# Kernel tuning notes

Hardware: AMD Instinct MI355X
Metric: run time of the kernel (lower is better)

## Reference

```python
import jax, jax.numpy as jnp
import numpy as np
import math

_B, _L, _D, _H = 4, 2048, 512, 8
_DH = _D // _H


def setup_inputs() -> dict:
    key = jax.random.key(0)
    ks = jax.random.split(key, 16)
    w_scale = 1.0 / math.sqrt(_D)
    def lin(kw, kb):
        W = jax.random.uniform(kw, (_D, _D), jnp.float32, -w_scale, w_scale)
        b = jax.random.uniform(kb, (_D,), jnp.float32, -w_scale, w_scale)
        return W, b
    Wq_w, Wq_b = lin(ks[0], ks[1])
    Wk_w, Wk_b = lin(ks[2], ks[3])
    Wv_w, Wv_b = lin(ks[4], ks[5])
    fc_w, fc_b = lin(ks[6], ks[7])
    Q = jax.random.normal(ks[8], (_B, _L, _D), jnp.float32)
    K = jax.random.normal(ks[9], (_B, _L, _D), jnp.float32)
    V = jax.random.normal(ks[10], (_B, _L, _D), jnp.float32)
    # E = torch.rand(L, DH): uniform [0,1), non-trainable buffer
    E = jax.random.uniform(ks[11], (_L, _DH), jnp.float32)
    # causal mask: True (1) where attention is disallowed -> gets -1e9
    mask = jnp.triu(jnp.ones((_L, _L), dtype=bool), k=1)[None, None]  # (1,1,L,L)
    return {"Q": Q, "K": K, "V": V, "mask": mask,
            "Wq_w": Wq_w, "Wq_b": Wq_b, "Wk_w": Wk_w, "Wk_b": Wk_b,
            "Wv_w": Wv_w, "Wv_b": Wv_b, "fc_w": fc_w, "fc_b": fc_b,
            "E": E, "H": _H}


def reference(Q, K, V, mask, Wq_w, Wq_b, Wk_w, Wk_b, Wv_w, Wv_b, fc_w, fc_b, E, H):
    B, Lq, D = Q.shape
    DH = D // H

    def proj(x, W, b):  # torch Linear: x @ W.T + b, then split heads -> (B,H,L,DH)
        y = x @ W.T + b
        return y.reshape(B, -1, H, DH).transpose(0, 2, 1, 3)

    q = proj(Q, Wq_w, Wq_b)
    k = proj(K, Wk_w, Wk_b)
    v = proj(V, Wv_w, Wv_b)
    Lk = k.shape[2]

    # _get_left_embedding: last Lq rows of E
    Eu = E[max(0, E.shape[0] - Lq):, :]            # (e, DH), e == Lq here
    e = Eu.shape[0]

    QE = jnp.einsum('bhld,ed->bhle', q, Eu)        # (B,H,Lq,e)
    # _qe_masking: keep QE[..., i, j] where j >= e-1-i (upper anti-triangle)
    i = jnp.arange(Lq)[:, None]
    j = jnp.arange(e)[None, :]
    keep = (i + j >= e - 1).astype(QE.dtype)
    QE = QE * keep

    # _skewing: pad one zero column, reshape, drop first row
    padded = jnp.pad(QE, ((0, 0), (0, 0), (0, 0), (1, 0)))   # (B,H,Lq,e+1)
    Srel = padded.reshape(B, H, e + 1, Lq)[:, :, 1:, :]      # (B,H,e,Lq)
    if Lk < Lq:
        Srel = Srel[:, :, :, :Lk]

    logits = (jnp.einsum('bhld,bhmd->bhlm', q, k) + Srel) / math.sqrt(DH)
    logits = logits + mask.astype(jnp.float32) * (-1e9)
    AW = jax.nn.softmax(logits, axis=-1)
    out = jnp.einsum('bhlm,bhmd->bhld', AW, v)               # (B,H,Lq,DH)
    out = out.transpose(0, 2, 1, 3).reshape(B, -1, D)        # (B,Lq,D)
    return out @ fc_w.T + fc_b
```

## Files before the change

### kernel.cpp

```cpp
#include <hip/hip_runtime.h>
#include <stdint.h>

typedef __bf16 bf16;
typedef float f32x4 __attribute__((ext_vector_type(4)));
typedef bf16 bf16x8 __attribute__((ext_vector_type(8)));
typedef bf16 bf16x4 __attribute__((ext_vector_type(4)));

#define MFMA16(a, b, c) __builtin_amdgcn_mfma_f32_16x16x32_bf16((a), (b), (c), 0, 0, 0)
#define EXP2F(x) __builtin_amdgcn_exp2f(x)

__device__ __forceinline__ void gll16(const void* g, void* l) {
  __builtin_amdgcn_global_load_lds((const __attribute__((address_space(1))) void*)g,
                                   (__attribute__((address_space(3))) void*)l, 16, 0, 0);
}

__global__ __launch_bounds__(256) void convert_all(
    const float4* __restrict__ Q, const float4* __restrict__ K, const float4* __restrict__ V,
    const float4* __restrict__ Wq, const float4* __restrict__ Wk, const float4* __restrict__ Wv,
    const float4* __restrict__ fcw, const float4* __restrict__ E,
    bf16x4* __restrict__ Xq, bf16x4* __restrict__ Xk, bf16x4* __restrict__ Xv,
    bf16x4* __restrict__ Wqb, bf16x4* __restrict__ Wkb, bf16x4* __restrict__ Wvb,
    bf16x4* __restrict__ fcb, bf16x4* __restrict__ Eb) {
  int i = blockIdx.x * 256 + threadIdx.x;
  const float4* s;
  bf16x4* d;
  int off;
  if (i < 1048576) { s = Q; d = Xq; off = i; }
  else if (i < 2097152) { s = K; d = Xk; off = i - 1048576; }
  else if (i < 3145728) { s = V; d = Xv; off = i - 2097152; }
  else if (i < 3211264) { s = Wq; d = Wqb; off = i - 3145728; }
  else if (i < 3276800) { s = Wk; d = Wkb; off = i - 3211264; }
  else if (i < 3342336) { s = Wv; d = Wvb; off = i - 3276800; }
  else if (i < 3407872) { s = fcw; d = fcb; off = i - 3342336; }
  else { s = E; d = Eb; off = i - 3407872; }
  float4 v = s[off];
  bf16x4 o;
  o[0] = (bf16)v.x; o[1] = (bf16)v.y; o[2] = (bf16)v.z; o[3] = (bf16)v.w;
  d[off] = o;
}

__device__ __forceinline__ void gemm_core(const bf16* __restrict__ A, const bf16* __restrict__ Bt,
                                          bf16* ldsA, bf16* ldsB, int m0, int n0,
                                          f32x4 acc[4][4]) {
  const int t = threadIdx.x;
  const int lane = t & 63, w = t >> 6;
  const int l15 = lane & 15, quad = lane >> 4;
  const int wm = w >> 1, wn = w & 1;
#pragma unroll
  for (int i = 0; i < 4; i++)
#pragma unroll
    for (int j = 0; j < 4; j++) acc[i][j] = (f32x4){0.f, 0.f, 0.f, 0.f};

  const int ch0 = t, ch1 = t + 256;
  const int r0 = ch0 >> 2, c0 = (ch0 & 3) ^ (r0 & 3);
  const int r1 = ch1 >> 2, c1 = (ch1 & 3) ^ (r1 & 3);

  int aoff[4], boff[4];
#pragma unroll
  for (int mt = 0; mt < 4; mt++) {
    int m = wm * 64 + mt * 16 + l15;
    aoff[mt] = (m << 6) + ((quad ^ (l15 & 3)) << 4);
    int n = wn * 64 + mt * 16 + l15;
    boff[mt] = (n << 6) + ((quad ^ (l15 & 3)) << 4);
  }
  bf16* ldsA1 = ldsA + w * 512;
  bf16* ldsA2 = ldsA + 2048 + w * 512;
  bf16* ldsB1 = ldsB + w * 512;
  bf16* ldsB2 = ldsB + 2048 + w * 512;

  for (int kt = 0; kt < 512; kt += 32) {
    gll16(A + (size_t)(m0 + r0) * 512 + kt + c0 * 8, ldsA1);
    gll16(A + (size_t)(m0 + r1) * 512 + kt + c1 * 8, ldsA2);
    gll16(Bt + (size_t)(n0 + r0) * 512 + kt + c0 * 8, ldsB1);
    gll16(Bt + (size_t)(n0 + r1) * 512 + kt + c1 * 8, ldsB2);
    __syncthreads();
    bf16x8 af[4], bfr[4];
#pragma unroll
    for (int mt = 0; mt < 4; mt++) af[mt] = *(const bf16x8*)((const char*)ldsA + aoff[mt]);
#pragma unroll
    for (int nt = 0; nt < 4; nt++) bfr[nt] = *(const bf16x8*)((const char*)ldsB + boff[nt]);
#pragma unroll
    for (int mt = 0; mt < 4; mt++)
#pragma unroll
      for (int nt = 0; nt < 4; nt++)
        acc[mt][nt] = MFMA16(af[mt], bfr[nt], acc[mt][nt]);
    __syncthreads();
  }
}

__global__ __launch_bounds__(256) void proj_gemm(
    const bf16* __restrict__ Xq, const bf16* __restrict__ Xk, const bf16* __restrict__ Xv,
    const bf16* __restrict__ Wq, const bf16* __restrict__ Wk, const bf16* __restrict__ Wv,
    const float* __restrict__ bq, const float* __restrict__ bk, const float* __restrict__ bv,
    bf16* __restrict__ qb, bf16* __restrict__ kb, bf16* __restrict__ vb) {
  __shared__ bf16 ldsA[128 * 32];
  __shared__ bf16 ldsB[128 * 32];
  const int z = blockIdx.z;
  const bf16* A = z == 0 ? Xq : (z == 1 ? Xk : Xv);
  const bf16* W = z == 0 ? Wq : (z == 1 ? Wk : Wv);
  const float* bias = z == 0 ? bq : (z == 1 ? bk : bv);
  bf16* out = z == 0 ? qb : (z == 1 ? kb : vb);
  const int m0 = blockIdx.x * 128, n0 = blockIdx.y * 128;
  f32x4 acc[4][4];
  gemm_core(A, W, ldsA, ldsB, m0, n0, acc);

  const int t = threadIdx.x;
  const int lane = t & 63, w = t >> 6;
  const int l15 = lane & 15, quad = lane >> 4;
  const int wm = w >> 1, wn = w & 1;
#pragma unroll
  for (int mt = 0; mt < 4; mt++)
#pragma unroll
    for (int nt = 0; nt < 4; nt++)
#pragma unroll
      for (int r = 0; r < 4; r++) {
        int gm = m0 + wm * 64 + mt * 16 + quad * 4 + r;
        int gn = n0 + wn * 64 + nt * 16 + l15;
        float v = acc[mt][nt][r] + bias[gn];
        int b = gm >> 11, l = gm & 2047, h = gn >> 6, d = gn & 63;
        out[(((size_t)(b * 8 + h)) * 2048 + l) * 64 + d] = (bf16)v;
      }
}

__global__ __launch_bounds__(256) void final_gemm(const bf16* __restrict__ A,
                                                  const bf16* __restrict__ W,
                                                  const float* __restrict__ bias,
                                                  float* __restrict__ out) {
  __shared__ bf16 ldsA[128 * 32];
  __shared__ bf16 ldsB[128 * 32];
  const int m0 = blockIdx.x * 128, n0 = blockIdx.y * 128;
  f32x4 acc[4][4];
  gemm_core(A, W, ldsA, ldsB, m0, n0, acc);

  const int t = threadIdx.x;
  const int lane = t & 63, w = t >> 6;
  const int l15 = lane & 15, quad = lane >> 4;
  const int wm = w >> 1, wn = w & 1;
#pragma unroll
  for (int mt = 0; mt < 4; mt++)
#pragma unroll
    for (int nt = 0; nt < 4; nt++)
#pragma unroll
      for (int r = 0; r < 4; r++) {
        int gm = m0 + wm * 64 + mt * 16 + quad * 4 + r;
        int gn = n0 + wn * 64 + nt * 16 + l15;
        out[(size_t)gm * 512 + gn] = acc[mt][nt][r] + bias[gn];
      }
}

__global__ __launch_bounds__(256) void transpose_v(const bf16* __restrict__ vbuf,
                                                   bf16* __restrict__ vT) {
  __shared__ bf16 tile[64][72];
  const int bh = blockIdx.y, l0 = blockIdx.x * 64;
  const bf16* src = vbuf + ((size_t)bh * 2048 + l0) * 64;
  bf16* dst = vT + (size_t)bh * 64 * 2048 + l0;
  const int t = threadIdx.x;
#pragma unroll
  for (int p = 0; p < 2; p++) {
    int ch = t + p * 256;
    int r = ch >> 3, c8 = ch & 7;
    *(bf16x8*)&tile[r][c8 * 8] = *(const bf16x8*)&src[(size_t)r * 64 + c8 * 8];
  }
  __syncthreads();
#pragma unroll
  for (int p = 0; p < 2; p++) {
    int ch = t + p * 256;
    int dr = ch >> 3, lc = ch & 7;
    bf16x8 v;
#pragma unroll
    for (int j = 0; j < 8; j++) v[j] = tile[lc * 8 + j][dr];
    *(bf16x8*)&dst[(size_t)dr * 2048 + lc * 8] = v;
  }
}

__global__ __launch_bounds__(256, 4) void attn_kernel(
    const bf16* __restrict__ qbuf, const bf16* __restrict__ kbuf,
    const bf16* __restrict__ vT, const bf16* __restrict__ Eb,
    bf16* __restrict__ attnb, bf16* __restrict__ Of1,
    float* __restrict__ Os0, float* __restrict__ Os1) {
  __shared__ bf16 Kl[64 * 64];
  __shared__ bf16 Vl[64 * 64];
  __shared__ bf16 Pl[4][16 * 72];
  const int t = threadIdx.x, w = t >> 6, lane = t & 63;
  const int l15 = lane & 15, quad = lane >> 4;
  const int x = blockIdx.x;
  const int bh = x & 31, job = x >> 5;
  int strip, jt0, jt1;
  bool isB;
  if (job < 16) {
    strip = 16 + job; jt0 = 0; jt1 = 16; isB = false;
  } else {
    int k = job - 16, i = k >> 1;
    if ((k & 1) == 0) { strip = 15 - i; jt0 = 0; jt1 = 16 - i; isB = false; }
    else { strip = 31 - i; jt0 = 16; jt1 = 32 - i; isB = true; }
  }
  const int i0 = strip * 64 + w * 16;
  bf16* Pw = Pl[w];
  const bf16* qh = qbuf + (size_t)bh * 2048 * 64;
  const bf16* kh = kbuf + (size_t)bh * 2048 * 64;
  const bf16* vh = vT + (size_t)bh * 64 * 2048;

  const int sr0 = t >> 3, sc0 = (t & 7) ^ (sr0 & 7);
  const int sr1 = sr0 + 32;
  const int wb0 = (t & 192) * 16;
  const int wb1 = 4096 + wb0;

  int bpaddr[4];
  bool loA[4];
#pragma unroll
  for (int r = 0; r < 4; r++) {
    int u = quad * 4 + r;
    bpaddr[r] = (((l15 + 15 - u) & 15) + 16 * quad) * 4;
    loA[r] = (l15 <= u);
  }

  bf16x8 aq0, aq1;
  {
    const bf16* qrow = qh + (size_t)(i0 + l15) * 64 + quad * 8;
    aq0 = *(const bf16x8*)qrow;
    aq1 = *(const bf16x8*)(qrow + 32);
  }
  bf16x8 ones;
#pragma unroll
  for (int j = 0; j < 8; j++) ones[j] = (bf16)1.0f;

  f32x4 O[4], Osum;
  Osum = (f32x4){0.f, 0.f, 0.f, 0.f};
#pragma unroll
  for (int i = 0; i < 4; i++) O[i] = (f32x4){0.f, 0.f, 0.f, 0.f};
  const float sc = 0.125f * 1.44269504088896f;
  const int ebase00 = 2047 - i0 - 15;

  float Bpc[4];
  {
    int er = ebase00 + jt0 * 64 + l15;
    er = er > 2047 ? 2047 : er;
    const bf16* erow = Eb + (size_t)er * 64 + quad * 8;
    bf16x8 e0 = *(const bf16x8*)erow;
    bf16x8 e1 = *(const bf16x8*)(erow + 32);
    f32x4 zz = (f32x4){0.f, 0.f, 0.f, 0.f};
    zz = MFMA16(aq0, e0, zz);
    zz = MFMA16(aq1, e1, zz);
#pragma unroll
    for (int r = 0; r < 4; r++)
      Bpc[r] = __int_as_float(__builtin_amdgcn_ds_bpermute(bpaddr[r], __float_as_int(zz[r])));
  }

  for (int jt = jt0; jt < jt1; jt++) {
    const int j0 = jt * 64;
    const bool diag = (jt == strip);
    __syncthreads();
    gll16(kh + (size_t)(j0 + sr0) * 64 + sc0 * 8, (char*)Kl + wb0);
    gll16(kh + (size_t)(j0 + sr1) * 64 + sc0 * 8, (char*)Kl + wb1);
    gll16(vh + (size_t)sr0 * 2048 + j0 + sc0 * 8, (char*)Vl + wb0);
    gll16(vh + (size_t)sr1 * 2048 + j0 + sc0 * 8, (char*)Vl + wb1);
    float Bp[5][4];
#pragma unroll
    for (int r = 0; r < 4; r++) Bp[0][r] = Bpc[r];
    const int ebase = ebase00 + j0;
#pragma unroll
    for (int nt = 1; nt < 5; nt++) {
      int er = ebase + nt * 16 + l15;
      er = er > 2047 ? 2047 : er;
      const bf16* erow = Eb + (size_t)er * 64 + quad * 8;
      bf16x8 e0 = *(const bf16x8*)erow;
      bf16x8 e1 = *(const bf16x8*)(erow + 32);
      f32x4 zz = (f32x4){0.f, 0.f, 0.f, 0.f};
      zz = MFMA16(aq0, e0, zz);
      zz = MFMA16(aq1, e1, zz);
#pragma unroll
      for (int r = 0; r < 4; r++)
        Bp[nt][r] =
            __int_as_float(__builtin_amdgcn_ds_bpermute(bpaddr[r], __float_as_int(zz[r])));
    }
#pragma unroll
    for (int r = 0; r < 4; r++) Bpc[r] = Bp[4][r];

    __syncthreads();
    f32x4 s[4];
#pragma unroll
    for (int nt = 0; nt < 4; nt++) {
      int row = nt * 16 + l15;
      bf16x8 k0 = *(const bf16x8*)(Kl + ((row << 3) + (quad ^ (row & 7))) * 8);
      bf16x8 k1 = *(const bf16x8*)(Kl + ((row << 3) + ((quad + 4) ^ (row & 7))) * 8);
      f32x4 zz = (f32x4){0.f, 0.f, 0.f, 0.f};
      zz = MFMA16(aq0, k0, zz);
      s[nt] = MFMA16(aq1, k1, zz);
    }
    if (diag) {
#pragma unroll
      for (int nt = 0; nt < 4; nt++)
#pragma unroll
        for (int r = 0; r < 4; r++) {
          int u = quad * 4 + r;
          int j = nt * 16 + l15;
          float skew = loA[r] ? Bp[nt][r] : Bp[nt + 1][r];
          float logit = (s[nt][r] + skew) * sc;
          if (j0 + j > i0 + u) logit = -1e30f;
          Pw[u * 72 + j] = (bf16)EXP2F(logit);
        }
    } else {
#pragma unroll
      for (int nt = 0; nt < 4; nt++)
#pragma unroll
        for (int r = 0; r < 4; r++) {
          int u = quad * 4 + r;
          int j = nt * 16 + l15;
          float skew = loA[r] ? Bp[nt][r] : Bp[nt + 1][r];
          Pw[u * 72 + j] = (bf16)EXP2F((s[nt][r] + skew) * sc);
        }
    }
    bf16x8 pa0 = *(const bf16x8*)&Pw[l15 * 72 + quad * 8];
    bf16x8 pa1 = *(const bf16x8*)&Pw[l15 * 72 + 32 + quad * 8];
    Osum = MFMA16(pa0, ones, Osum);
    Osum = MFMA16(pa1, ones, Osum);
#pragma unroll
    for (int nt = 0; nt < 4; nt++) {
      int row = nt * 16 + l15;
      bf16x8 v0 = *(const bf16x8*)(Vl + ((row << 3) + (quad ^ (row & 7))) * 8);
      bf16x8 v1 = *(const bf16x8*)(Vl + ((row << 3) + ((quad + 4) ^ (row & 7))) * 8);
      O[nt] = MFMA16(pa0, v0, O[nt]);
      O[nt] = MFMA16(pa1, v1, O[nt]);
    }
  }
  if (isB) {
    bf16* orow = Of1 + ((size_t)(bh * 1024 + (i0 - 1024))) * 64;
#pragma unroll
    for (int nt = 0; nt < 4; nt++)
#pragma unroll
      for (int r = 0; r < 4; r++)
        orow[(size_t)(quad * 4 + r) * 64 + nt * 16 + l15] = (bf16)O[nt][r];
    if (l15 == 0) {
#pragma unroll
      for (int r = 0; r < 4; r++) Os1[bh * 1024 + (i0 - 1024) + quad * 4 + r] = Osum[r];
    }
  } else {
    const int b = bh >> 3, hh = bh & 7;
    bf16* orow = attnb + ((size_t)(b * 2048 + i0)) * 512 + hh * 64;
#pragma unroll
    for (int nt = 0; nt < 4; nt++)
#pragma unroll
      for (int r = 0; r < 4; r++)
        orow[(size_t)(quad * 4 + r) * 512 + nt * 16 + l15] = (bf16)O[nt][r];
    if (l15 == 0) {
#pragma unroll
      for (int r = 0; r < 4; r++) Os0[bh * 2048 + i0 + quad * 4 + r] = Osum[r];
    }
  }
}

__global__ __launch_bounds__(256) void norm_kernel(bf16x8* __restrict__ attnb,
                                                   const bf16x8* __restrict__ Of1,
                                                   const float* __restrict__ Os0,
                                                   const float* __restrict__ Os1) {
  int i = blockIdx.x * 256 + threadIdx.x;
  int col8 = i & 63;
  int row = i >> 6;
  int b = row >> 11, l = row & 2047, h = col8 >> 3;
  int bh = b * 8 + h;
  float s = Os0[bh * 2048 + l];
  bf16x8 v0 = attnb[i];
  float acc[8];
#pragma unroll
  for (int j = 0; j < 8; j++) acc[j] = (float)v0[j];
  if (l >= 1024) {
    s += Os1[bh * 1024 + l - 1024];
    bf16x8 v1 = Of1[(size_t)(bh * 1024 + l - 1024) * 8 + (col8 & 7)];
#pragma unroll
    for (int j = 0; j < 8; j++) acc[j] += (float)v1[j];
  }
  float inv = 1.0f / s;
  bf16x8 o;
#pragma unroll
  for (int j = 0; j < 8; j++) o[j] = (bf16)(acc[j] * inv);
  attnb[i] = o;
}

extern "C" void kernel_launch(void* const* d_in, const int* in_sizes, int n_in,
                              void* d_out, int out_size, void* d_ws, size_t ws_size,
                              hipStream_t stream) {
  const float* Q = (const float*)d_in[0];
  const float* K = (const float*)d_in[1];
  const float* V = (const float*)d_in[2];
  const float* Wq = (const float*)d_in[4];
  const float* bq = (const float*)d_in[5];
  const float* Wk = (const float*)d_in[6];
  const float* bk = (const float*)d_in[7];
  const float* Wv = (const float*)d_in[8];
  const float* bv = (const float*)d_in[9];
  const float* fcw = (const float*)d_in[10];
  const float* fcb = (const float*)d_in[11];
  const float* E = (const float*)d_in[12];

  char* ws = (char*)d_ws;
  bf16* Xq = (bf16*)(ws + 0);
  bf16* Xk = (bf16*)(ws + 8388608);
  bf16* Xv = (bf16*)(ws + 16777216);
  bf16* Wqb = (bf16*)(ws + 25165824);
  bf16* Wkb = (bf16*)(ws + 25690112);
  bf16* Wvb = (bf16*)(ws + 26214400);
  bf16* fcwb = (bf16*)(ws + 26738688);
  bf16* Eb = (bf16*)(ws + 27262976);
  bf16* qbuf = (bf16*)(ws + 27525120);
  bf16* kbuf = (bf16*)(ws + 35913728);
  bf16* vbuf = (bf16*)(ws + 44302336);
  bf16* Of1 = (bf16*)(ws + 52690944);
  float* Os0 = (float*)(ws + 56885248);
  float* Os1 = (float*)(ws + 57147392);
  bf16* vTb = Xk;
  bf16* attnb = Xq;

  convert_all<<<13440, 256, 0, stream>>>(
      (const float4*)Q, (const float4*)K, (const float4*)V, (const float4*)Wq,
      (const float4*)Wk, (const float4*)Wv, (const float4*)fcw, (const float4*)E,
      (bf16x4*)Xq, (bf16x4*)Xk, (bf16x4*)Xv, (bf16x4*)Wqb, (bf16x4*)Wkb,
      (bf16x4*)Wvb, (bf16x4*)fcwb, (bf16x4*)Eb);

  proj_gemm<<<dim3(64, 4, 3), 256, 0, stream>>>(Xq, Xk, Xv, Wqb, Wkb, Wvb, bq, bk, bv,
                                                qbuf, kbuf, vbuf);

  transpose_v<<<dim3(32, 32), 256, 0, stream>>>(vbuf, vTb);

  attn_kernel<<<1536, 256, 0, stream>>>(qbuf, kbuf, vTb, Eb, attnb, Of1, Os0, Os1);

  norm_kernel<<<2048, 256, 0, stream>>>((bf16x8*)attnb, (const bf16x8*)Of1, Os0, Os1);

  final_gemm<<<dim3(64, 4, 1), 256, 0, stream>>>(attnb, fcwb, fcb, (float*)d_out);
}
```

Baseline: 247.9 us.

## Fuse fp32-to-bf16 conversion into GEMM tile loads and add MFMA priority hints

The standalone conversion pass over Q, K, V and the weights is removed. The projection and output GEMMs now load fp32 tiles straight into LDS, using a swizzled layout with twice the bytes per tile, and convert to bf16 when reading fragments. This drops a full extra read and write of the activations in exchange for more LDS traffic and conversion work inside the GEMM loop. The attention kernel also raises wave priority around its MFMA sections using s_setprio.

```diff
diff --git a/kernel.cpp b/kernel.cpp
--- a/kernel.cpp
+++ b/kernel.cpp
@@ -14,34 +14,19 @@
                                    (__attribute__((address_space(3))) void*)l, 16, 0, 0);
 }
 
-__global__ __launch_bounds__(256) void convert_all(
-    const float4* __restrict__ Q, const float4* __restrict__ K, const float4* __restrict__ V,
-    const float4* __restrict__ Wq, const float4* __restrict__ Wk, const float4* __restrict__ Wv,
-    const float4* __restrict__ fcw, const float4* __restrict__ E,
-    bf16x4* __restrict__ Xq, bf16x4* __restrict__ Xk, bf16x4* __restrict__ Xv,
-    bf16x4* __restrict__ Wqb, bf16x4* __restrict__ Wkb, bf16x4* __restrict__ Wvb,
-    bf16x4* __restrict__ fcb, bf16x4* __restrict__ Eb) {
+__global__ __launch_bounds__(256) void convert_E(const float4* __restrict__ E,
+                                                 bf16x4* __restrict__ Eb) {
   int i = blockIdx.x * 256 + threadIdx.x;
-  const float4* s;
-  bf16x4* d;
-  int off;
-  if (i < 1048576) { s = Q; d = Xq; off = i; }
-  else if (i < 2097152) { s = K; d = Xk; off = i - 1048576; }
-  else if (i < 3145728) { s = V; d = Xv; off = i - 2097152; }
-  else if (i < 3211264) { s = Wq; d = Wqb; off = i - 3145728; }
-  else if (i < 3276800) { s = Wk; d = Wkb; off = i - 3211264; }
-  else if (i < 3342336) { s = Wv; d = Wvb; off = i - 3276800; }
-  else if (i < 3407872) { s = fcw; d = fcb; off = i - 3342336; }
-  else { s = E; d = Eb; off = i - 3407872; }
-  float4 v = s[off];
+  float4 v = E[i];
   bf16x4 o;
   o[0] = (bf16)v.x; o[1] = (bf16)v.y; o[2] = (bf16)v.z; o[3] = (bf16)v.w;
-  d[off] = o;
-}
-
-__device__ __forceinline__ void gemm_core(const bf16* __restrict__ A, const bf16* __restrict__ Bt,
-                                          bf16* ldsA, bf16* ldsB, int m0, int n0,
-                                          f32x4 acc[4][4]) {
+  Eb[i] = o;
+}
+
+template <bool AF32, bool BF32>
+__device__ __forceinline__ void gemm_core_t(const void* __restrict__ Ap,
+                                            const void* __restrict__ Bp, char* ldsA,
+                                            char* ldsB, int m0, int n0, f32x4 acc[4][4]) {
   const int t = threadIdx.x;
   const int lane = t & 63, w = t >> 6;
   const int l15 = lane & 15, quad = lane >> 4;
@@ -51,34 +36,75 @@
 #pragma unroll
     for (int j = 0; j < 4; j++) acc[i][j] = (f32x4){0.f, 0.f, 0.f, 0.f};
 
-  const int ch0 = t, ch1 = t + 256;
-  const int r0 = ch0 >> 2, c0 = (ch0 & 3) ^ (r0 & 3);
-  const int r1 = ch1 >> 2, c1 = (ch1 & 3) ^ (r1 & 3);
-
-  int aoff[4], boff[4];
-#pragma unroll
-  for (int mt = 0; mt < 4; mt++) {
-    int m = wm * 64 + mt * 16 + l15;
-    aoff[mt] = (m << 6) + ((quad ^ (l15 & 3)) << 4);
-    int n = wn * 64 + mt * 16 + l15;
-    boff[mt] = (n << 6) + ((quad ^ (l15 & 3)) << 4);
-  }
-  bf16* ldsA1 = ldsA + w * 512;
-  bf16* ldsA2 = ldsA + 2048 + w * 512;
-  bf16* ldsB1 = ldsB + w * 512;
-  bf16* ldsB2 = ldsB + 2048 + w * 512;
+  const int wbase = (t & 192) * 16;
 
   for (int kt = 0; kt < 512; kt += 32) {
-    gll16(A + (size_t)(m0 + r0) * 512 + kt + c0 * 8, ldsA1);
-    gll16(A + (size_t)(m0 + r1) * 512 + kt + c1 * 8, ldsA2);
-    gll16(Bt + (size_t)(n0 + r0) * 512 + kt + c0 * 8, ldsB1);
-    gll16(Bt + (size_t)(n0 + r1) * 512 + kt + c1 * 8, ldsB2);
+    if constexpr (AF32) {
+      const float* A = (const float*)Ap;
+#pragma unroll
+      for (int p = 0; p < 4; p++) {
+        int ch = t + 256 * p;
+        int r = ch >> 3, c = (ch & 7) ^ (r & 7);
+        gll16(A + (size_t)(m0 + r) * 512 + kt + c * 4, ldsA + p * 4096 + wbase);
+      }
+    } else {
+      const bf16* A = (const bf16*)Ap;
+#pragma unroll
+      for (int p = 0; p < 2; p++) {
+        int ch = t + 256 * p;
+        int r = ch >> 2, c = (ch & 3) ^ (r & 3);
+        gll16(A + (size_t)(m0 + r) * 512 + kt + c * 8, ldsA + p * 4096 + wbase);
+      }
+    }
+    if constexpr (BF32) {
+      const float* B = (const float*)Bp;
+#pragma unroll
+      for (int p = 0; p < 4; p++) {
+        int ch = t + 256 * p;
+        int r = ch >> 3, c = (ch & 7) ^ (r & 7);
+        gll16(B + (size_t)(n0 + r) * 512 + kt + c * 4, ldsB + p * 4096 + wbase);
+      }
+    } else {
+      const bf16* B = (const bf16*)Bp;
+#pragma unroll
+      for (int p = 0; p < 2; p++) {
+        int ch = t + 256 * p;
+        int r = ch >> 2, c = (ch & 3) ^ (r & 3);
+        gll16(B + (size_t)(n0 + r) * 512 + kt + c * 8, ldsB + p * 4096 + wbase);
+      }
+    }
     __syncthreads();
     bf16x8 af[4], bfr[4];
 #pragma unroll
-    for (int mt = 0; mt < 4; mt++) af[mt] = *(const bf16x8*)((const char*)ldsA + aoff[mt]);
-#pragma unroll
-    for (int nt = 0; nt < 4; nt++) bfr[nt] = *(const bf16x8*)((const char*)ldsB + boff[nt]);
+    for (int mt = 0; mt < 4; mt++) {
+      int m = wm * 64 + mt * 16 + l15;
+      if constexpr (AF32) {
+        const char* base = ldsA + (m << 7);
+        float4 x0 = *(const float4*)(base + ((((quad << 1) | 0) ^ (m & 7)) << 4));
+        float4 x1 = *(const float4*)(base + ((((quad << 1) | 1) ^ (m & 7)) << 4));
+        bf16x8 v;
+        v[0] = (bf16)x0.x; v[1] = (bf16)x0.y; v[2] = (bf16)x0.z; v[3] = (bf16)x0.w;
+        v[4] = (bf16)x1.x; v[5] = (bf16)x1.y; v[6] = (bf16)x1.z; v[7] = (bf16)x1.w;
+        af[mt] = v;
+      } else {
+        af[mt] = *(const bf16x8*)(ldsA + (m << 6) + ((quad ^ (m & 3)) << 4));
+      }
+    }
+#pragma unroll
+    for (int nt = 0; nt < 4; nt++) {
+      int n = wn * 64 + nt * 16 + l15;
+      if constexpr (BF32) {
+        const char* base = ldsB + (n << 7);
+        float4 x0 = *(const float4*)(base + ((((quad << 1) | 0) ^ (n & 7)) << 4));
+        float4 x1 = *(const float4*)(base + ((((quad << 1) | 1) ^ (n & 7)) << 4));
+        bf16x8 v;
+        v[0] = (bf16)x0.x; v[1] = (bf16)x0.y; v[2] = (bf16)x0.z; v[3] = (bf16)x0.w;
+        v[4] = (bf16)x1.x; v[5] = (bf16)x1.y; v[6] = (bf16)x1.z; v[7] = (bf16)x1.w;
+        bfr[nt] = v;
+      } else {
+        bfr[nt] = *(const bf16x8*)(ldsB + (n << 6) + ((quad ^ (n & 3)) << 4));
+      }
+    }
 #pragma unroll
     for (int mt = 0; mt < 4; mt++)
 #pragma unroll
@@ -89,20 +115,20 @@
 }
 
 __global__ __launch_bounds__(256) void proj_gemm(
-    const bf16* __restrict__ Xq, const bf16* __restrict__ Xk, const bf16* __restrict__ Xv,
-    const bf16* __restrict__ Wq, const bf16* __restrict__ Wk, const bf16* __restrict__ Wv,
+    const float* __restrict__ Xq, const float* __restrict__ Xk, const float* __restrict__ Xv,
+    const float* __restrict__ Wq, const float* __restrict__ Wk, const float* __restrict__ Wv,
     const float* __restrict__ bq, const float* __restrict__ bk, const float* __restrict__ bv,
     bf16* __restrict__ qb, bf16* __restrict__ kb, bf16* __restrict__ vb) {
-  __shared__ bf16 ldsA[128 * 32];
-  __shared__ bf16 ldsB[128 * 32];
+  __shared__ __align__(16) char ldsA[16384];
+  __shared__ __align__(16) char ldsB[16384];
   const int z = blockIdx.z;
-  const bf16* A = z == 0 ? Xq : (z == 1 ? Xk : Xv);
-  const bf16* W = z == 0 ? Wq : (z == 1 ? Wk : Wv);
+  const float* A = z == 0 ? Xq : (z == 1 ? Xk : Xv);
+  const float* W = z == 0 ? Wq : (z == 1 ? Wk : Wv);
   const float* bias = z == 0 ? bq : (z == 1 ? bk : bv);
   bf16* out = z == 0 ? qb : (z == 1 ? kb : vb);
   const int m0 = blockIdx.x * 128, n0 = blockIdx.y * 128;
   f32x4 acc[4][4];
-  gemm_core(A, W, ldsA, ldsB, m0, n0, acc);
+  gemm_core_t<true, true>(A, W, ldsA, ldsB, m0, n0, acc);
 
   const int t = threadIdx.x;
   const int lane = t & 63, w = t >> 6;
@@ -123,14 +149,14 @@
 }
 
 __global__ __launch_bounds__(256) void final_gemm(const bf16* __restrict__ A,
-                                                  const bf16* __restrict__ W,
+                                                  const float* __restrict__ W,
                                                   const float* __restrict__ bias,
                                                   float* __restrict__ out) {
-  __shared__ bf16 ldsA[128 * 32];
-  __shared__ bf16 ldsB[128 * 32];
+  __shared__ __align__(16) char ldsA[8192];
+  __shared__ __align__(16) char ldsB[16384];
   const int m0 = blockIdx.x * 128, n0 = blockIdx.y * 128;
   f32x4 acc[4][4];
-  gemm_core(A, W, ldsA, ldsB, m0, n0, acc);
+  gemm_core_t<false, true>(A, W, ldsA, ldsB, m0, n0, acc);
 
   const int t = threadIdx.x;
   const int lane = t & 63, w = t >> 6;
@@ -277,6 +303,7 @@
     for (int r = 0; r < 4; r++) Bpc[r] = Bp[4][r];
 
     __syncthreads();
+    __builtin_amdgcn_s_setprio(1);
     f32x4 s[4];
 #pragma unroll
     for (int nt = 0; nt < 4; nt++) {
@@ -287,6 +314,7 @@
       zz = MFMA16(aq0, k0, zz);
       s[nt] = MFMA16(aq1, k1, zz);
     }
+    __builtin_amdgcn_s_setprio(0);
     if (diag) {
 #pragma unroll
       for (int nt = 0; nt < 4; nt++)
@@ -312,6 +340,7 @@
     }
     bf16x8 pa0 = *(const bf16x8*)&Pw[l15 * 72 + quad * 8];
     bf16x8 pa1 = *(const bf16x8*)&Pw[l15 * 72 + 32 + quad * 8];
+    __builtin_amdgcn_s_setprio(1);
     Osum = MFMA16(pa0, ones, Osum);
     Osum = MFMA16(pa1, ones, Osum);
 #pragma unroll
@@ -322,6 +351,7 @@
       O[nt] = MFMA16(pa0, v0, O[nt]);
       O[nt] = MFMA16(pa1, v1, O[nt]);
     }
+    __builtin_amdgcn_s_setprio(0);
   }
   if (isB) {
     bf16* orow = Of1 + ((size_t)(bh * 1024 + (i0 - 1024))) * 64;
@@ -393,13 +423,6 @@
   const float* E = (const float*)d_in[12];
 
   char* ws = (char*)d_ws;
-  bf16* Xq = (bf16*)(ws + 0);
-  bf16* Xk = (bf16*)(ws + 8388608);
-  bf16* Xv = (bf16*)(ws + 16777216);
-  bf16* Wqb = (bf16*)(ws + 25165824);
-  bf16* Wkb = (bf16*)(ws + 25690112);
-  bf16* Wvb = (bf16*)(ws + 26214400);
-  bf16* fcwb = (bf16*)(ws + 26738688);
   bf16* Eb = (bf16*)(ws + 27262976);
   bf16* qbuf = (bf16*)(ws + 27525120);
   bf16* kbuf = (bf16*)(ws + 35913728);
@@ -407,16 +430,12 @@
   bf16* Of1 = (bf16*)(ws + 52690944);
   float* Os0 = (float*)(ws + 56885248);
   float* Os1 = (float*)(ws + 57147392);
-  bf16* vTb = Xk;
-  bf16* attnb = Xq;
-
-  convert_all<<<13440, 256, 0, stream>>>(
-      (const float4*)Q, (const float4*)K, (const float4*)V, (const float4*)Wq,
-      (const float4*)Wk, (const float4*)Wv, (const float4*)fcw, (const float4*)E,
-      (bf16x4*)Xq, (bf16x4*)Xk, (bf16x4*)Xv, (bf16x4*)Wqb, (bf16x4*)Wkb,
-      (bf16x4*)Wvb, (bf16x4*)fcwb, (bf16x4*)Eb);
-
-  proj_gemm<<<dim3(64, 4, 3), 256, 0, stream>>>(Xq, Xk, Xv, Wqb, Wkb, Wvb, bq, bk, bv,
+  bf16* vTb = (bf16*)(ws + 8388608);
+  bf16* attnb = (bf16*)(ws + 0);
+
+  convert_E<<<128, 256, 0, stream>>>((const float4*)E, (bf16x4*)Eb);
+
+  proj_gemm<<<dim3(64, 4, 3), 256, 0, stream>>>(Q, K, V, Wq, Wk, Wv, bq, bk, bv,
                                                 qbuf, kbuf, vbuf);
 
   transpose_v<<<dim3(32, 32), 256, 0, stream>>>(vbuf, vTb);
@@ -425,5 +444,5 @@
 
   norm_kernel<<<2048, 256, 0, stream>>>((bf16x8*)attnb, (const bf16x8*)Of1, Os0, Os1);
 
-  final_gemm<<<dim3(64, 4, 1), 256, 0, stream>>>(attnb, fcwb, fcb, (float*)d_out);
-}
+  final_gemm<<<dim3(64, 4, 1), 256, 0, stream>>>(attnb, fcw, fcb, (float*)d_out);
+}
```

Result: slower. 267.0 us (+7.7%).
